# Kernel optimization log

Measured on AMD Instinct MI355X. Metric: run time of the kernel, lower is better.

## Reference

```python
import jax, jax.numpy as jnp
import numpy as np

N = 20000   # nodes
E = 320000  # edges (avg degree 16)
K = 3       # Chebyshev order


def _glorot(key, shape):
    fan_in, fan_out = shape[-2], shape[-1]
    lim = (6.0 / (fan_in + fan_out)) ** 0.5
    return jax.random.uniform(key, shape, minval=-lim, maxval=lim, dtype=jnp.float32)


def setup_inputs() -> dict:
    key = jax.random.key(0)
    ks = jax.random.split(key, 8)
    v = jax.random.normal(ks[0], (N, 86), dtype=jnp.float32)
    edges = jax.random.randint(ks[1], (2, E), 0, N, dtype=jnp.int32)
    W1 = _glorot(ks[2], (K, 86, 128));  b1 = jnp.zeros((128,), jnp.float32)
    W2 = _glorot(ks[3], (K, 128, 256)); b2 = jnp.zeros((256,), jnp.float32)
    W3 = _glorot(ks[4], (K, 256, 512)); b3 = jnp.zeros((512,), jnp.float32)
    return {"v": v, "edges": edges, "W1": W1, "b1": b1,
            "W2": W2, "b2": b2, "W3": W3, "b3": b3}


def _cheb_norm(edges, n):
    # PyG ChebConv with sym norm, lambda_max=2: L_hat = L - I = -D^-1/2 A D^-1/2
    # (diagonal entries from get_laplacian (+1) and add_self_loops (-1) cancel).
    # Self loops are removed before computing the Laplacian -> mask them out.
    row, col = edges[0], edges[1]
    w = (row != col).astype(jnp.float32)
    deg = jax.ops.segment_sum(w, row, num_segments=n)
    dinv = jnp.where(deg > 0, jax.lax.rsqrt(jnp.maximum(deg, 1e-12)), 0.0)
    norm_w = -dinv[row] * w * dinv[col]  # [E]
    return row, col, norm_w


def _cheb_conv(x, row, col, norm_w, W, b):
    # W: [K, in, out]
    def prop(z):  # L_hat @ z via edge gather + segment scatter-add
        return jax.ops.segment_sum(norm_w[:, None] * z[col], row, num_segments=x.shape[0])
    Tx0 = x
    out = Tx0 @ W[0]
    Tx1 = prop(Tx0)
    out = out + Tx1 @ W[1]
    Tx2 = 2.0 * prop(Tx1) - Tx0
    out = out + Tx2 @ W[2]
    return out + b


def reference(v, edges, W1, b1, W2, b2, W3, b3):
    row, col, norm_w = _cheb_norm(edges, v.shape[0])
    nk = jax.random.key(42)
    x1 = jax.nn.relu(_cheb_conv(v, row, col, norm_w, W1, b1))
    x1 = x1 * jax.random.normal(jax.random.fold_in(nk, 1), x1.shape, x1.dtype)
    x2 = jax.nn.relu(_cheb_conv(x1, row, col, norm_w, W2, b2))
    x2 = x2 * jax.random.normal(jax.random.fold_in(nk, 2), x2.shape, x2.dtype)
    x3 = jax.nn.relu(_cheb_conv(x2, row, col, norm_w, W3, b3))
    x3 = x3 * jax.random.normal(jax.random.fold_in(nk, 3), x3.shape, x3.dtype)
    return (x1, x2, x3)
```

## Files before the change

kernel.cpp:

```cpp
#include <hip/hip_runtime.h>
#include <stdint.h>
#include <math.h>

#define DEV static __device__ __forceinline__

typedef __attribute__((ext_vector_type(8))) short bf16x8;
typedef __attribute__((ext_vector_type(4))) float f32x4;
typedef __attribute__((ext_vector_type(8))) unsigned short u16x8;

DEV uint32_t rotl32(uint32_t v, int d) { return (v << d) | (v >> (32 - d)); }

DEV void threefry2x32(uint32_t k0, uint32_t k1, uint32_t& x0, uint32_t& x1) {
  const uint32_t k2 = k0 ^ k1 ^ 0x1BD11BDAu;
  x0 += k0; x1 += k1;
#define TFR(R) { x0 += x1; x1 = rotl32(x1, R) ^ x0; }
  TFR(13) TFR(15) TFR(26) TFR(6)
  x0 += k1; x1 += k2 + 1u;
  TFR(17) TFR(29) TFR(16) TFR(24)
  x0 += k2; x1 += k0 + 2u;
  TFR(13) TFR(15) TFR(26) TFR(6)
  x0 += k0; x1 += k1 + 3u;
  TFR(17) TFR(29) TFR(16) TFR(24)
  x0 += k1; x1 += k2 + 4u;
  TFR(13) TFR(15) TFR(26) TFR(6)
  x0 += k2; x1 += k0 + 5u;
#undef TFR
}

DEV float erfinv_f32(float x) {
  float w = -log1pf(-x * x);
  float p;
  if (w < 5.0f) {
    w -= 2.5f;
    p = 2.81022636e-08f;
    p = fmaf(p, w, 3.43273939e-07f);
    p = fmaf(p, w, -3.5233877e-06f);
    p = fmaf(p, w, -4.39150654e-06f);
    p = fmaf(p, w, 0.00021858087f);
    p = fmaf(p, w, -0.00125372503f);
    p = fmaf(p, w, -0.00417768164f);
    p = fmaf(p, w, 0.246640727f);
    p = fmaf(p, w, 1.50140941f);
  } else {
    w = sqrtf(w) - 3.0f;
    p = -0.000200214257f;
    p = fmaf(p, w, 0.000100950558f);
    p = fmaf(p, w, 0.00134934322f);
    p = fmaf(p, w, -0.00367342844f);
    p = fmaf(p, w, 0.00573950773f);
    p = fmaf(p, w, -0.0076224613f);
    p = fmaf(p, w, 0.00943887047f);
    p = fmaf(p, w, 1.00167406f);
    p = fmaf(p, w, 2.83297682f);
  }
  return p * x;
}

DEV float normal_from_bits(uint32_t bits) {
  float f = __uint_as_float((bits >> 9) | 0x3F800000u) - 1.0f;
  const float lo = -0.99999994f;
  float u = fmaf(f, 2.0f, lo);
  u = fmaxf(u, lo);
  return 1.41421356f * erfinv_f32(u);
}

DEV unsigned short f2bf(float f) {
  uint32_t u = __float_as_uint(f);
  uint32_t r = u + 0x7FFFu + ((u >> 16) & 1u);
  return (unsigned short)(r >> 16);
}

DEV float bf2f(uint32_t h) { return __uint_as_float(h << 16); }

__global__ void count_kernel(const int* __restrict__ rows, const int* __restrict__ cols,
                             int* __restrict__ counts, int* __restrict__ degs, int E) {
  int e = blockIdx.x * blockDim.x + threadIdx.x;
  if (e < E) {
    int r = rows[e];
    atomicAdd(&counts[r], 1);
    if (r != cols[e]) atomicAdd(&degs[r], 1);
  }
}

__global__ void dinv_kernel(const int* __restrict__ degs, float* __restrict__ dinv, int N) {
  int i = blockIdx.x * blockDim.x + threadIdx.x;
  if (i < N) {
    int d = degs[i];
    dinv[i] = d > 0 ? rsqrtf((float)d) : 0.0f;
  }
}

#define SCAN_T 1024
__global__ __launch_bounds__(SCAN_T) void scan_kernel(const int* __restrict__ counts,
                                                      int* __restrict__ row_ptr,
                                                      int* __restrict__ cursor, int N) {
  __shared__ int sa[SCAN_T], sb[SCAN_T];
  const int t = threadIdx.x;
  const int CH = (N + SCAN_T - 1) / SCAN_T;
  int base = t * CH;
  int psum = 0;
  for (int k = 0; k < CH; ++k) {
    int idx = base + k;
    if (idx < N) psum += counts[idx];
  }
  sa[t] = psum;
  __syncthreads();
  int* src = sa; int* dst = sb;
  for (int off = 1; off < SCAN_T; off <<= 1) {
    int v = src[t];
    if (t >= off) v += src[t - off];
    dst[t] = v;
    __syncthreads();
    int* tmp = src; src = dst; dst = tmp;
  }
  int running = src[t] - psum;
  for (int k = 0; k < CH; ++k) {
    int idx = base + k;
    if (idx < N) {
      row_ptr[idx] = running;
      cursor[idx] = running;
      running += counts[idx];
    }
  }
  if (t == SCAN_T - 1) row_ptr[N] = running;
}

__global__ void fill_kernel(const int* __restrict__ rows, const int* __restrict__ cols,
                            const float* __restrict__ dinv, int* __restrict__ cursor,
                            float2* __restrict__ ecv, int E) {
  int e = blockIdx.x * blockDim.x + threadIdx.x;
  if (e < E) {
    int r = rows[e], c = cols[e];
    float w = (r != c) ? -dinv[r] * dinv[c] : 0.0f;
    int pos = atomicAdd(&cursor[r], 1);
    ecv[pos] = make_float2(__int_as_float(c), w);
  }
}

template <int VEC>
DEV void ldrow(const unsigned short* base, size_t off, float* v) {
  const unsigned short* p = base + off;
  if (VEC == 4) {
    uint2 u = *(const uint2*)p;
    v[0] = bf2f(u.x & 0xffffu); v[1] = bf2f(u.x >> 16);
    v[2] = bf2f(u.y & 0xffffu); v[3] = bf2f(u.y >> 16);
  } else {
    uint32_t u = *(const uint32_t*)p;
    v[0] = bf2f(u & 0xffffu); v[1] = bf2f(u >> 16);
  }
}

template <int VEC, int SUB>
__global__ __launch_bounds__(256) void gather_prop(
    const int* __restrict__ row_ptr, const float2* __restrict__ ecv,
    const unsigned short* __restrict__ xsrc, int sstride,
    const float* __restrict__ xsub, int substride,
    unsigned short* __restrict__ outb, int N, int F, int Fpad) {
  const int wave = threadIdx.x >> 6, lane = threadIdx.x & 63;
  const int node = blockIdx.x * 4 + wave;
  if (node >= N) return;
  const int f0 = lane * VEC;
  if (f0 >= Fpad) return;
  const bool live = (f0 + VEC) <= F;
  float acc[VEC] = {};
  if (live) {
    const int s = row_ptr[node], e = row_ptr[node + 1];
    int j = s;
    for (; j + 8 <= e; j += 8) {
      float2 cw[8];
      float vv[8][VEC];
#pragma unroll
      for (int q = 0; q < 8; ++q) cw[q] = ecv[j + q];
#pragma unroll
      for (int q = 0; q < 8; ++q)
        ldrow<VEC>(xsrc, (size_t)__float_as_int(cw[q].x) * sstride + f0, vv[q]);
#pragma unroll
      for (int q = 0; q < 8; ++q)
#pragma unroll
        for (int z = 0; z < VEC; ++z) acc[z] = fmaf(cw[q].y, vv[q][z], acc[z]);
    }
    for (; j < e; ++j) {
      float2 cw = ecv[j];
      float vv[VEC];
      ldrow<VEC>(xsrc, (size_t)__float_as_int(cw.x) * sstride + f0, vv);
#pragma unroll
      for (int z = 0; z < VEC; ++z) acc[z] = fmaf(cw.y, vv[z], acc[z]);
    }
    if (SUB) {
      const float* sb = xsub + (size_t)node * substride + f0;
#pragma unroll
      for (int z = 0; z < VEC; ++z) acc[z] = fmaf(2.0f, acc[z], -sb[z]);
    }
  }
  size_t ob = (size_t)node * Fpad + f0;
  if (VEC == 4) {
    uint2 u;
    u.x = (uint32_t)f2bf(acc[0]) | ((uint32_t)f2bf(acc[1]) << 16);
    u.y = (uint32_t)f2bf(acc[2]) | ((uint32_t)f2bf(acc[3]) << 16);
    *(uint2*)&outb[ob] = u;
  } else {
    uint32_t u = (uint32_t)f2bf(acc[0]) | ((uint32_t)f2bf(acc[1]) << 16);
    *(uint32_t*)&outb[ob] = u;
  }
}

__global__ void wtrans_kernel(const float* __restrict__ W, unsigned short* __restrict__ Wt,
                              int F, int Fpad, int O) {
  int idx = blockIdx.x * 256 + threadIdx.x;
  int total = 3 * O * Fpad;
  if (idx >= total) return;
  int k = idx % Fpad;
  int o = (idx / Fpad) % O;
  int p = idx / (Fpad * O);
  Wt[idx] = (k < F) ? f2bf(W[((size_t)p * F + k) * O + o]) : (unsigned short)0;
}

__global__ void vconv_kernel(const float* __restrict__ v, unsigned short* __restrict__ vb, int N) {
  int i = blockIdx.x * 256 + threadIdx.x;
  if (i >= N * 96) return;
  int r = i / 96, k = i % 96;
  vb[i] = (k < 86) ? f2bf(v[(size_t)r * 86 + k]) : (unsigned short)0;
}

template <int BM, int FPAD, int KS>
__global__ __launch_bounds__(512, 4) void gemm3_db(
    const unsigned short* __restrict__ A0, const unsigned short* __restrict__ A1,
    const unsigned short* __restrict__ A2,
    const unsigned short* __restrict__ Wt, const float* __restrict__ bias,
    int M, int O, float* __restrict__ out, unsigned short* __restrict__ outb,
    int obstride, int fold) {
  constexpr int BN = 128;
  constexpr int NSP = FPAD / KS;
  constexpr int NSTEP = 3 * NSP;
  constexpr int CPR = KS / 8;
  constexpr int LST = KS + 8;
  constexpr int NA = BM * CPR;
  constexpr int NB = BN * CPR;
  constexpr int ACH = (NA + 511) / 512;
  constexpr int BCH = (NB + 511) / 512;
  constexpr int MFR = BM / 32;
  constexpr int KK = KS / 32;

  __shared__ unsigned short sA[2][BM * LST];
  __shared__ unsigned short sB[2][BN * LST];

  const int tid = threadIdx.x;
  const int lane = tid & 63;
  const int wave = tid >> 6;
  const int wm = wave >> 2, wo = wave & 3;
  const int bm = blockIdx.x * BM;
  const int bo = blockIdx.y * BN;
  const int l15 = lane & 15;
  const int kg = (lane >> 4) * 8;

  f32x4 acc[MFR][2] = {};
  const unsigned short* As[3] = {A0, A1, A2};

  u16x8 ra[ACH], rb[BCH];

  auto issue = [&](int s) {
    int p = s / NSP, k0 = (s % NSP) * KS;
    const unsigned short* __restrict__ A = As[p];
    const unsigned short* __restrict__ B = Wt + (size_t)p * O * FPAD;
#pragma unroll
    for (int c = 0; c < ACH; ++c) {
      int idx = tid + c * 512;
      if (NA % 512 == 0 || idx < NA) {
        int row = idx / CPR, ch = (idx % CPR) * 8;
        int gm = bm + row; if (gm >= M) gm = M - 1;
        ra[c] = *(const u16x8*)(A + (size_t)gm * FPAD + k0 + ch);
      }
    }
#pragma unroll
    for (int c = 0; c < BCH; ++c) {
      int idx = tid + c * 512;
      if (NB % 512 == 0 || idx < NB) {
        int row = idx / CPR, ch = (idx % CPR) * 8;
        rb[c] = *(const u16x8*)(B + (size_t)(bo + row) * FPAD + k0 + ch);
      }
    }
  };

  auto lds_write = [&](int buf) {
#pragma unroll
    for (int c = 0; c < ACH; ++c) {
      int idx = tid + c * 512;
      if (NA % 512 == 0 || idx < NA) {
        int row = idx / CPR, ch = (idx % CPR) * 8;
        *(u16x8*)&sA[buf][row * LST + ch] = ra[c];
      }
    }
#pragma unroll
    for (int c = 0; c < BCH; ++c) {
      int idx = tid + c * 512;
      if (NB % 512 == 0 || idx < NB) {
        int row = idx / CPR, ch = (idx % CPR) * 8;
        *(u16x8*)&sB[buf][row * LST + ch] = rb[c];
      }
    }
  };

  auto compute = [&](int buf) {
#pragma unroll
    for (int kk = 0; kk < KK; ++kk) {
      bf16x8 af[MFR], bfr[2];
#pragma unroll
      for (int mi = 0; mi < MFR; ++mi)
        af[mi] = *(const bf16x8*)&sA[buf][(wm * (BM / 2) + mi * 16 + l15) * LST + kk * 32 + kg];
#pragma unroll
      for (int ni = 0; ni < 2; ++ni)
        bfr[ni] = *(const bf16x8*)&sB[buf][(wo * 32 + ni * 16 + l15) * LST + kk * 32 + kg];
#pragma unroll
      for (int mi = 0; mi < MFR; ++mi)
#pragma unroll
        for (int ni = 0; ni < 2; ++ni)
          acc[mi][ni] = __builtin_amdgcn_mfma_f32_16x16x32_bf16(af[mi], bfr[ni], acc[mi][ni], 0, 0, 0);
    }
  };

  issue(0);
  lds_write(0);
  __syncthreads();

  int cur = 0;
#pragma unroll
  for (int s = 0; s < NSTEP; ++s) {
    if (s + 1 < NSTEP) issue(s + 1);
    compute(cur);
    if (s + 1 < NSTEP) {
      lds_write(cur ^ 1);
      __syncthreads();
      cur ^= 1;
    }
  }

  uint32_t f0 = 0u, f1 = (uint32_t)fold;
  threefry2x32(0u, 42u, f0, f1);
  const int r0 = (lane >> 4) * 4;
#pragma unroll
  for (int mi = 0; mi < MFR; ++mi) {
#pragma unroll
    for (int r = 0; r < 4; ++r) {
      int gm = bm + wm * (BM / 2) + mi * 16 + r0 + r;
      if (gm >= M) continue;
#pragma unroll
      for (int ni = 0; ni < 2; ++ni) {
        int go = bo + wo * 32 + ni * 16 + l15;
        float vv = acc[mi][ni][r] + bias[go];
        vv = vv > 0.0f ? vv : 0.0f;
        uint32_t a = 0u, b = (uint32_t)(gm * O + go);
        threefry2x32(f0, f1, a, b);
        float res = vv * normal_from_bits(a ^ b);
        out[(size_t)gm * O + go] = res;
        if (outb) outb[(size_t)gm * obstride + go] = f2bf(res);
      }
    }
  }
}

extern "C" void kernel_launch(void* const* d_in, const int* in_sizes, int n_in,
                              void* d_out, int out_size, void* d_ws, size_t ws_size,
                              hipStream_t stream) {
  const float* v    = (const float*)d_in[0];
  const int*  edges = (const int*)d_in[1];
  const float* W1 = (const float*)d_in[2];
  const float* b1 = (const float*)d_in[3];
  const float* W2 = (const float*)d_in[4];
  const float* b2 = (const float*)d_in[5];
  const float* W3 = (const float*)d_in[6];
  const float* b3 = (const float*)d_in[7];
  float* out = (float*)d_out;

  const int N = in_sizes[0] / 86;
  const int E = in_sizes[1] / 2;
  const int* rows = edges;
  const int* cols = edges + E;

  uintptr_t cur = (uintptr_t)d_ws;
  auto alloc = [&](size_t bytes) {
    cur = (cur + 15) & ~(uintptr_t)15;
    void* p = (void*)cur;
    cur += bytes;
    return p;
  };
  float2* ecv          = (float2*)alloc((size_t)E * 8);
  int* counts          = (int*)alloc((size_t)N * 4);
  int* degs            = (int*)alloc((size_t)N * 4);
  int* row_ptr         = (int*)alloc((size_t)(N + 1) * 4);
  int* cursor          = (int*)alloc((size_t)N * 4);
  float* dinv          = (float*)alloc((size_t)N * 4);
  unsigned short* tx1b = (unsigned short*)alloc((size_t)N * 256 * 2);
  unsigned short* tx2b = (unsigned short*)alloc((size_t)N * 256 * 2);
  unsigned short* vb   = (unsigned short*)alloc((size_t)N * 96 * 2);
  unsigned short* x1b  = (unsigned short*)alloc((size_t)N * 128 * 2);
  unsigned short* x2b  = (unsigned short*)alloc((size_t)N * 256 * 2);
  unsigned short* Wt   = (unsigned short*)alloc((size_t)3 * 512 * 256 * 2);

  float* x1 = out;
  float* x2 = x1 + (size_t)N * 128;
  float* x3 = x2 + (size_t)N * 256;

  hipMemsetAsync(counts, 0, (size_t)2 * N * sizeof(int), stream);
  count_kernel<<<(E + 255) / 256, 256, 0, stream>>>(rows, cols, counts, degs, E);
  dinv_kernel<<<(N + 255) / 256, 256, 0, stream>>>(degs, dinv, N);
  scan_kernel<<<1, SCAN_T, 0, stream>>>(counts, row_ptr, cursor, N);
  fill_kernel<<<(E + 255) / 256, 256, 0, stream>>>(rows, cols, dinv, cursor, ecv, E);
  vconv_kernel<<<(N * 96 + 255) / 256, 256, 0, stream>>>(v, vb, N);

  const int pblocks = (N + 3) / 4;

  {
    wtrans_kernel<<<(3 * 128 * 96 + 255) / 256, 256, 0, stream>>>(W1, Wt, 86, 96, 128);
    gather_prop<2, 0><<<pblocks, 256, 0, stream>>>(row_ptr, ecv, vb, 96, nullptr, 0, tx1b, N, 86, 96);
    gather_prop<2, 1><<<pblocks, 256, 0, stream>>>(row_ptr, ecv, tx1b, 96, v, 86, tx2b, N, 86, 96);
    dim3 g((N + 63) / 64, 1);
    gemm3_db<64, 96, 32><<<g, 512, 0, stream>>>(vb, tx1b, tx2b, Wt, b1, N, 128, x1, x1b, 128, 1);
  }
  {
    wtrans_kernel<<<(3 * 256 * 128 + 255) / 256, 256, 0, stream>>>(W2, Wt, 128, 128, 256);
    gather_prop<2, 0><<<pblocks, 256, 0, stream>>>(row_ptr, ecv, x1b, 128, nullptr, 0, tx1b, N, 128, 128);
    gather_prop<2, 1><<<pblocks, 256, 0, stream>>>(row_ptr, ecv, tx1b, 128, x1, 128, tx2b, N, 128, 128);
    dim3 g((N + 127) / 128, 2);
    gemm3_db<128, 128, 64><<<g, 512, 0, stream>>>(x1b, tx1b, tx2b, Wt, b2, N, 256, x2, x2b, 256, 2);
  }
  {
    wtrans_kernel<<<(3 * 512 * 256 + 255) / 256, 256, 0, stream>>>(W3, Wt, 256, 256, 512);
    gather_prop<4, 0><<<pblocks, 256, 0, stream>>>(row_ptr, ecv, x2b, 256, nullptr, 0, tx1b, N, 256, 256);
    gather_prop<4, 1><<<pblocks, 256, 0, stream>>>(row_ptr, ecv, tx1b, 256, x2, 256, tx2b, N, 256, 256);
    dim3 g((N + 127) / 128, 4);
    gemm3_db<128, 256, 64><<<g, 512, 0, stream>>>(x2b, tx1b, tx2b, Wt, b3, N, 512, x3, nullptr, 0, 3);
  }
}
```

Baseline: 408.0 us.

## Precompute noise in separate kernel, fold dinv into fill, widen gather unroll

Moves threefry noise generation out of the GEMM epilogue into a separate noise_kernel that writes a full fp32 noise buffer, which the GEMM then reads. It also removes the dinv kernel by computing rsqrt of the degrees inside fill_kernel, and raises the gather edge unroll to 16 or 12 with a 4-wide tail loop. The aim is to lighten the GEMM epilogue and cut a launch, at the cost of extra global memory traffic for the noise buffer (up to N*512 floats written and read) and higher register pressure in the gather kernels.

New measurement: 405.2 us. No clear change (-0.7%).

```diff
diff --git a/kernel.cpp b/kernel.cpp
--- a/kernel.cpp
+++ b/kernel.cpp
@@ -82,14 +82,6 @@
   }
 }
 
-__global__ void dinv_kernel(const int* __restrict__ degs, float* __restrict__ dinv, int N) {
-  int i = blockIdx.x * blockDim.x + threadIdx.x;
-  if (i < N) {
-    int d = degs[i];
-    dinv[i] = d > 0 ? rsqrtf((float)d) : 0.0f;
-  }
-}
-
 #define SCAN_T 1024
 __global__ __launch_bounds__(SCAN_T) void scan_kernel(const int* __restrict__ counts,
                                                       int* __restrict__ row_ptr,
@@ -126,12 +118,13 @@
 }
 
 __global__ void fill_kernel(const int* __restrict__ rows, const int* __restrict__ cols,
-                            const float* __restrict__ dinv, int* __restrict__ cursor,
+                            const int* __restrict__ degs, int* __restrict__ cursor,
                             float2* __restrict__ ecv, int E) {
   int e = blockIdx.x * blockDim.x + threadIdx.x;
   if (e < E) {
     int r = rows[e], c = cols[e];
-    float w = (r != c) ? -dinv[r] * dinv[c] : 0.0f;
+    int dr = degs[r], dc = degs[c];
+    float w = (r != c && dr > 0 && dc > 0) ? -rsqrtf((float)dr) * rsqrtf((float)dc) : 0.0f;
     int pos = atomicAdd(&cursor[r], 1);
     ecv[pos] = make_float2(__int_as_float(c), w);
   }
@@ -150,7 +143,7 @@
   }
 }
 
-template <int VEC, int SUB>
+template <int VEC, int SUB, int U>
 __global__ __launch_bounds__(256) void gather_prop(
     const int* __restrict__ row_ptr, const float2* __restrict__ ecv,
     const unsigned short* __restrict__ xsrc, int sstride,
@@ -166,16 +159,29 @@
   if (live) {
     const int s = row_ptr[node], e = row_ptr[node + 1];
     int j = s;
-    for (; j + 8 <= e; j += 8) {
-      float2 cw[8];
-      float vv[8][VEC];
-#pragma unroll
-      for (int q = 0; q < 8; ++q) cw[q] = ecv[j + q];
-#pragma unroll
-      for (int q = 0; q < 8; ++q)
+    for (; j + U <= e; j += U) {
+      float2 cw[U];
+      float vv[U][VEC];
+#pragma unroll
+      for (int q = 0; q < U; ++q) cw[q] = ecv[j + q];
+#pragma unroll
+      for (int q = 0; q < U; ++q)
         ldrow<VEC>(xsrc, (size_t)__float_as_int(cw[q].x) * sstride + f0, vv[q]);
 #pragma unroll
-      for (int q = 0; q < 8; ++q)
+      for (int q = 0; q < U; ++q)
+#pragma unroll
+        for (int z = 0; z < VEC; ++z) acc[z] = fmaf(cw[q].y, vv[q][z], acc[z]);
+    }
+    for (; j + 4 <= e; j += 4) {
+      float2 cw[4];
+      float vv[4][VEC];
+#pragma unroll
+      for (int q = 0; q < 4; ++q) cw[q] = ecv[j + q];
+#pragma unroll
+      for (int q = 0; q < 4; ++q)
+        ldrow<VEC>(xsrc, (size_t)__float_as_int(cw[q].x) * sstride + f0, vv[q]);
+#pragma unroll
+      for (int q = 0; q < 4; ++q)
 #pragma unroll
         for (int z = 0; z < VEC; ++z) acc[z] = fmaf(cw[q].y, vv[q][z], acc[z]);
     }
@@ -222,13 +228,37 @@
   vb[i] = (k < 86) ? f2bf(v[(size_t)r * 86 + k]) : (unsigned short)0;
 }
 
+template <int FOLD>
+__global__ __launch_bounds__(256) void noise_kernel(float* __restrict__ nb, int total4) {
+  uint32_t f0 = 0u, f1 = (uint32_t)FOLD;
+  threefry2x32(0u, 42u, f0, f1);
+  int i4 = blockIdx.x * 256 + threadIdx.x;
+  if (i4 >= total4) return;
+  uint32_t base = (uint32_t)i4 * 4u;
+  float4 r;
+  {
+    uint32_t a = 0u, b = base + 0u; threefry2x32(f0, f1, a, b); r.x = normal_from_bits(a ^ b);
+  }
+  {
+    uint32_t a = 0u, b = base + 1u; threefry2x32(f0, f1, a, b); r.y = normal_from_bits(a ^ b);
+  }
+  {
+    uint32_t a = 0u, b = base + 2u; threefry2x32(f0, f1, a, b); r.z = normal_from_bits(a ^ b);
+  }
+  {
+    uint32_t a = 0u, b = base + 3u; threefry2x32(f0, f1, a, b); r.w = normal_from_bits(a ^ b);
+  }
+  *(float4*)&nb[(size_t)base] = r;
+}
+
 template <int BM, int FPAD, int KS>
 __global__ __launch_bounds__(512, 4) void gemm3_db(
     const unsigned short* __restrict__ A0, const unsigned short* __restrict__ A1,
     const unsigned short* __restrict__ A2,
     const unsigned short* __restrict__ Wt, const float* __restrict__ bias,
+    const float* __restrict__ noise,
     int M, int O, float* __restrict__ out, unsigned short* __restrict__ outb,
-    int obstride, int fold) {
+    int obstride) {
   constexpr int BN = 128;
   constexpr int NSP = FPAD / KS;
   constexpr int NSTEP = 3 * NSP;
@@ -334,8 +364,6 @@
     }
   }
 
-  uint32_t f0 = 0u, f1 = (uint32_t)fold;
-  threefry2x32(0u, 42u, f0, f1);
   const int r0 = (lane >> 4) * 4;
 #pragma unroll
   for (int mi = 0; mi < MFR; ++mi) {
@@ -348,9 +376,7 @@
         int go = bo + wo * 32 + ni * 16 + l15;
         float vv = acc[mi][ni][r] + bias[go];
         vv = vv > 0.0f ? vv : 0.0f;
-        uint32_t a = 0u, b = (uint32_t)(gm * O + go);
-        threefry2x32(f0, f1, a, b);
-        float res = vv * normal_from_bits(a ^ b);
+        float res = vv * noise[(size_t)gm * O + go];
         out[(size_t)gm * O + go] = res;
         if (outb) outb[(size_t)gm * obstride + go] = f2bf(res);
       }
@@ -388,13 +414,13 @@
   int* degs            = (int*)alloc((size_t)N * 4);
   int* row_ptr         = (int*)alloc((size_t)(N + 1) * 4);
   int* cursor          = (int*)alloc((size_t)N * 4);
-  float* dinv          = (float*)alloc((size_t)N * 4);
   unsigned short* tx1b = (unsigned short*)alloc((size_t)N * 256 * 2);
   unsigned short* tx2b = (unsigned short*)alloc((size_t)N * 256 * 2);
   unsigned short* vb   = (unsigned short*)alloc((size_t)N * 96 * 2);
   unsigned short* x1b  = (unsigned short*)alloc((size_t)N * 128 * 2);
   unsigned short* x2b  = (unsigned short*)alloc((size_t)N * 256 * 2);
   unsigned short* Wt   = (unsigned short*)alloc((size_t)3 * 512 * 256 * 2);
+  float* nbuf          = (float*)alloc((size_t)N * 512 * 4);
 
   float* x1 = out;
   float* x2 = x1 + (size_t)N * 128;
@@ -402,32 +428,37 @@
 
   hipMemsetAsync(counts, 0, (size_t)2 * N * sizeof(int), stream);
   count_kernel<<<(E + 255) / 256, 256, 0, stream>>>(rows, cols, counts, degs, E);
-  dinv_kernel<<<(N + 255) / 256, 256, 0, stream>>>(degs, dinv, N);
   scan_kernel<<<1, SCAN_T, 0, stream>>>(counts, row_ptr, cursor, N);
-  fill_kernel<<<(E + 255) / 256, 256, 0, stream>>>(rows, cols, dinv, cursor, ecv, E);
+  fill_kernel<<<(E + 255) / 256, 256, 0, stream>>>(rows, cols, degs, cursor, ecv, E);
   vconv_kernel<<<(N * 96 + 255) / 256, 256, 0, stream>>>(v, vb, N);
 
   const int pblocks = (N + 3) / 4;
 
   {
     wtrans_kernel<<<(3 * 128 * 96 + 255) / 256, 256, 0, stream>>>(W1, Wt, 86, 96, 128);
-    gather_prop<2, 0><<<pblocks, 256, 0, stream>>>(row_ptr, ecv, vb, 96, nullptr, 0, tx1b, N, 86, 96);
-    gather_prop<2, 1><<<pblocks, 256, 0, stream>>>(row_ptr, ecv, tx1b, 96, v, 86, tx2b, N, 86, 96);
+    gather_prop<2, 0, 16><<<pblocks, 256, 0, stream>>>(row_ptr, ecv, vb, 96, nullptr, 0, tx1b, N, 86, 96);
+    gather_prop<2, 1, 16><<<pblocks, 256, 0, stream>>>(row_ptr, ecv, tx1b, 96, v, 86, tx2b, N, 86, 96);
+    int t4 = N * 128 / 4;
+    noise_kernel<1><<<(t4 + 255) / 256, 256, 0, stream>>>(nbuf, t4);
     dim3 g((N + 63) / 64, 1);
-    gemm3_db<64, 96, 32><<<g, 512, 0, stream>>>(vb, tx1b, tx2b, Wt, b1, N, 128, x1, x1b, 128, 1);
+    gemm3_db<64, 96, 32><<<g, 512, 0, stream>>>(vb, tx1b, tx2b, Wt, b1, nbuf, N, 128, x1, x1b, 128);
   }
   {
     wtrans_kernel<<<(3 * 256 * 128 + 255) / 256, 256, 0, stream>>>(W2, Wt, 128, 128, 256);
-    gather_prop<2, 0><<<pblocks, 256, 0, stream>>>(row_ptr, ecv, x1b, 128, nullptr, 0, tx1b, N, 128, 128);
-    gather_prop<2, 1><<<pblocks, 256, 0, stream>>>(row_ptr, ecv, tx1b, 128, x1, 128, tx2b, N, 128, 128);
+    gather_prop<2, 0, 16><<<pblocks, 256, 0, stream>>>(row_ptr, ecv, x1b, 128, nullptr, 0, tx1b, N, 128, 128);
+    gather_prop<2, 1, 16><<<pblocks, 256, 0, stream>>>(row_ptr, ecv, tx1b, 128, x1, 128, tx2b, N, 128, 128);
+    int t4 = N * 256 / 4;
+    noise_kernel<2><<<(t4 + 255) / 256, 256, 0, stream>>>(nbuf, t4);
     dim3 g((N + 127) / 128, 2);
-    gemm3_db<128, 128, 64><<<g, 512, 0, stream>>>(x1b, tx1b, tx2b, Wt, b2, N, 256, x2, x2b, 256, 2);
+    gemm3_db<128, 128, 64><<<g, 512, 0, stream>>>(x1b, tx1b, tx2b, Wt, b2, nbuf, N, 256, x2, x2b, 256);
   }
   {
     wtrans_kernel<<<(3 * 512 * 256 + 255) / 256, 256, 0, stream>>>(W3, Wt, 256, 256, 512);
-    gather_prop<4, 0><<<pblocks, 256, 0, stream>>>(row_ptr, ecv, x2b, 256, nullptr, 0, tx1b, N, 256, 256);
-    gather_prop<4, 1><<<pblocks, 256, 0, stream>>>(row_ptr, ecv, tx1b, 256, x2, 256, tx2b, N, 256, 256);
+    gather_prop<4, 0, 12><<<pblocks, 256, 0, stream>>>(row_ptr, ecv, x2b, 256, nullptr, 0, tx1b, N, 256, 256);
+    gather_prop<4, 1, 12><<<pblocks, 256, 0, stream>>>(row_ptr, ecv, tx1b, 256, x2, 256, tx2b, N, 256, 256);
+    int t4 = N * 512 / 4;
+    noise_kernel<3><<<(t4 + 255) / 256, 256, 0, stream>>>(nbuf, t4);
     dim3 g((N + 127) / 128, 4);
-    gemm3_db<128, 256, 64><<<g, 512, 0, stream>>>(x2b, tx1b, tx2b, Wt, b3, N, 512, x3, nullptr, 0, 3);
-  }
-}
+    gemm3_db<128, 256, 64><<<g, 512, 0, stream>>>(x2b, tx1b, tx2b, Wt, b3, nbuf, N, 512, x3, nullptr, 0);
+  }
+}
```
